# Kernel optimization log

Measured on AMD Instinct MI355X. Metric: run time of the kernel, lower is better.

The kernel has to match this reference:

```python
import jax, jax.numpy as jnp
import numpy as np

NEG_SLOPE = 0.2

def gatv2(x, edge_index, Wl, bl, Wr, br, att, bias):
    # PyG GATv2Conv (share_weights=False, add_self_loops=True, concat=True)
    N = x.shape[0]
    H, D = att.shape
    src0, dst0 = edge_index[0], edge_index[1]
    # remove_self_loops + add_self_loops semantics: mask existing self loops,
    # append one self loop per node (keeps static shapes under jit)
    loop = jnp.arange(N, dtype=src0.dtype)
    src = jnp.concatenate([src0, loop])
    dst = jnp.concatenate([dst0, loop])
    keep = jnp.concatenate([src0 != dst0, jnp.ones(N, dtype=bool)])  # drop original i->i edges
    xl = (x @ Wl + bl).reshape(N, H, D)  # source-side transform
    xr = (x @ Wr + br).reshape(N, H, D)  # target-side transform
    e = xl[src] + xr[dst]                                  # [E,H,D]
    logits = jnp.einsum('ehd,hd->eh', jax.nn.leaky_relu(e, NEG_SLOPE), att)
    logits = jnp.where(keep[:, None], logits, -jnp.inf)
    m = jax.ops.segment_max(logits, dst, num_segments=N)   # [N,H]
    ex = jnp.where(keep[:, None], jnp.exp(logits - m[dst]), 0.0)
    denom = jax.ops.segment_sum(ex, dst, num_segments=N)   # [N,H]
    alpha = ex / (denom[dst] + 1e-16)                      # [E,H]
    out = jax.ops.segment_sum(alpha[..., None] * xl[src], dst, num_segments=N)
    return out.reshape(N, H * D) + bias

def setup_inputs() -> dict:
    key = jax.random.key(0)
    ks = jax.random.split(key, 20)
    N, E, F, Hd = 50000, 400000, 5, 128
    s = 0.05
    inp = {
        'x': jax.random.normal(ks[0], (N, F), dtype=jnp.float32),
        'edge_index': jax.random.randint(ks[1], (2, E), 0, N, dtype=jnp.int64),
        # node_embed MLP
        'W1': jax.random.normal(ks[2], (F, Hd), dtype=jnp.float32) * s,
        'b1': jnp.zeros((Hd,), jnp.float32),
        'W2': jax.random.normal(ks[3], (Hd, Hd), dtype=jnp.float32) * s,
        'b2': jnp.zeros((Hd,), jnp.float32),
        # gnn1: GATv2Conv(128 -> 128, heads=4)
        'Wl1': jax.random.normal(ks[4], (Hd, 4 * Hd), dtype=jnp.float32) * s,
        'bl1': jnp.zeros((4 * Hd,), jnp.float32),
        'Wr1': jax.random.normal(ks[5], (Hd, 4 * Hd), dtype=jnp.float32) * s,
        'br1': jnp.zeros((4 * Hd,), jnp.float32),
        'att1': jax.random.normal(ks[6], (4, Hd), dtype=jnp.float32) * s,
        'bias1': jnp.zeros((4 * Hd,), jnp.float32),
        # gnn2: GATv2Conv(512 -> 128, heads=1)
        'Wl2': jax.random.normal(ks[7], (4 * Hd, Hd), dtype=jnp.float32) * s,
        'bl2': jnp.zeros((Hd,), jnp.float32),
        'Wr2': jax.random.normal(ks[8], (4 * Hd, Hd), dtype=jnp.float32) * s,
        'br2': jnp.zeros((Hd,), jnp.float32),
        'att2': jax.random.normal(ks[9], (1, Hd), dtype=jnp.float32) * s,
        'bias2': jnp.zeros((Hd,), jnp.float32),
    }
    return inp

def reference(x, edge_index, W1, b1, W2, b2, Wl1, bl1, Wr1, br1, att1, bias1,
              Wl2, bl2, Wr2, br2, att2, bias2):
    h = jax.nn.relu(x @ W1 + b1) @ W2 + b2                 # node_embed MLP
    h = jax.nn.relu(gatv2(h, edge_index, Wl1, bl1, Wr1, br1, att1, bias1))
    out = gatv2(h, edge_index, Wl2, bl2, Wr2, br2, att2, bias2)
    return out  # [N, 128]
```

## Files before the change

kernel.cpp:

```cpp
#include <hip/hip_runtime.h>
#include <math.h>

typedef __attribute__((ext_vector_type(8))) short bf16x8;
typedef __attribute__((ext_vector_type(4))) float f32x4;
typedef unsigned short ushort;

static __device__ __forceinline__ ushort f2bf(float f) {
    unsigned u = __float_as_uint(f);
    u = u + 0x7fff + ((u >> 16) & 1);
    return (ushort)(u >> 16);
}
static __device__ __forceinline__ float bf2f(ushort h) {
    return __uint_as_float(((unsigned)h) << 16);
}


__global__ void k_init(int* __restrict__ counts, int N) {
    int i = blockIdx.x * blockDim.x + threadIdx.x;
    if (i < N) counts[i] = 1;
}

__global__ void k_count(const int* __restrict__ src, const int* __restrict__ dst,
                        int E, int* __restrict__ counts) {
    int e = blockIdx.x * blockDim.x + threadIdx.x;
    if (e < E) {
        int s = src[e], d = dst[e];
        if (s != d) atomicAdd(&counts[d], 1);
    }
}

__global__ __launch_bounds__(256) void k_blocksum(const int* __restrict__ counts, int N,
                                                  int* __restrict__ bsum) {
    __shared__ int s[256];
    int t = threadIdx.x, i = blockIdx.x * 256 + t;
    s[t] = (i < N) ? counts[i] : 0;
    __syncthreads();
    for (int off = 128; off > 0; off >>= 1) {
        if (t < off) s[t] += s[t + off];
        __syncthreads();
    }
    if (t == 0) bsum[blockIdx.x] = s[0];
}

__global__ __launch_bounds__(256) void k_scanblocks(const int* __restrict__ bsum, int NB,
                                                    int* __restrict__ boff,
                                                    int* __restrict__ rowptr, int N) {
    __shared__ int s[256];
    int t = threadIdx.x;
    int v = (t < NB) ? bsum[t] : 0;
    s[t] = v;
    __syncthreads();
    for (int off = 1; off < 256; off <<= 1) {
        int u = (t >= off) ? s[t - off] : 0;
        __syncthreads();
        s[t] += u;
        __syncthreads();
    }
    if (t < NB) boff[t] = s[t] - v;
    if (t == NB - 1) rowptr[N] = s[t];
}

__global__ __launch_bounds__(256) void k_scatter(const int* __restrict__ counts, int N,
                                                 const int* __restrict__ boff,
                                                 int* __restrict__ rowptr,
                                                 int* __restrict__ cursor) {
    __shared__ int s[256];
    int t = threadIdx.x, i = blockIdx.x * 256 + t;
    int c = (i < N) ? counts[i] : 0;
    s[t] = c;
    __syncthreads();
    for (int off = 1; off < 256; off <<= 1) {
        int u = (t >= off) ? s[t - off] : 0;
        __syncthreads();
        s[t] += u;
        __syncthreads();
    }
    if (i < N) {
        int excl = boff[blockIdx.x] + s[t] - c;
        rowptr[i] = excl;
        cursor[i] = excl;
    }
}

__global__ void k_fill(const int* __restrict__ src, const int* __restrict__ dst,
                       int E, int N, int* __restrict__ cursor, int* __restrict__ colA) {
    int i = blockIdx.x * blockDim.x + threadIdx.x;
    if (i < E) {
        int s = src[i], d = dst[i];
        if (s != d) { int p = atomicAdd(&cursor[d], 1); colA[p] = s; }
    } else if (i < E + N) {
        int n = i - E;
        int p = atomicAdd(&cursor[n], 1); colA[p] = n;
    }
}


__global__ __launch_bounds__(256) void k_repack(
    const float* __restrict__ W2, const float* __restrict__ Wl1,
    const float* __restrict__ Wr1, const float* __restrict__ Wl2,
    const float* __restrict__ Wr2,
    ushort* __restrict__ wfh, ushort* __restrict__ wfl)
{
    int job = blockIdx.y;
    int t = blockIdx.x * 256 + threadIdx.x;
    int ks = t >> 9, n = (t >> 6) & 7, l = t & 63;

    const float* W; int ldw, rowoff, col0;
    if (job == 0)      { W = W2;  ldw = 128; rowoff = 0;              col0 = 0; }
    else if (job < 5)  { W = Wl1; ldw = 512; rowoff = 0;              col0 = (job - 1) * 128; }
    else if (job < 9)  { W = Wr1; ldw = 512; rowoff = 0;              col0 = (job - 5) * 128; }
    else if (job < 13) { W = Wl2; ldw = 128; rowoff = (job - 9) * 128;  col0 = 0; }
    else               { W = Wr2; ldw = 128; rowoff = (job - 13) * 128; col0 = 0; }

    int krow = rowoff + ks * 32 + (l >> 4) * 8;
    int col = col0 + n * 16 + (l & 15);
    size_t dbase = (size_t)job * 16384 + (((size_t)(ks * 8 + n)) * 64 + l) * 8;
#pragma unroll
    for (int j = 0; j < 8; j++) {
        float v = W[(size_t)(krow + j) * ldw + col];
        ushort h = f2bf(v);
        ushort lo = f2bf(v - bf2f(h));
        wfh[dbase + j] = h;
        wfl[dbase + j] = lo;
    }
}


__global__ __launch_bounds__(256) void k_mlp1(
    const float* __restrict__ x, const float* __restrict__ W1, const float* __restrict__ b1,
    ushort* __restrict__ outh, ushort* __restrict__ outl, int N)
{
    int n = blockIdx.x * 2 + (threadIdx.x >> 7);
    int j = threadIdx.x & 127;
    if (n >= N) return;
    float s = b1[j];
#pragma unroll
    for (int k = 0; k < 5; k++) s = fmaf(x[(size_t)n * 5 + k], W1[k * 128 + j], s);
    s = fmaxf(s, 0.f);
    ushort h = f2bf(s);
    outh[(size_t)n * 128 + j] = h;
    outl[(size_t)n * 128 + j] = f2bf(s - bf2f(h));
}


__global__ __launch_bounds__(256) void gemm_mfma(
    const ushort* __restrict__ Ah, const ushort* __restrict__ Al,
    const ushort* __restrict__ wfh, const ushort* __restrict__ wfl,
    const float* __restrict__ bias,
    ushort* __restrict__ Ch, ushort* __restrict__ Cl,
    int M)
{
    int tid = threadIdx.x;
    int w = tid >> 6, l = tid & 63;
    int m0 = blockIdx.x * 128 + w * 32;
    int lr = l & 15, kg = l >> 4;

    f32x4 acc[2][8];
#pragma unroll
    for (int i = 0; i < 2; i++)
#pragma unroll
        for (int j = 0; j < 8; j++) acc[i][j] = (f32x4){0.f, 0.f, 0.f, 0.f};

    int row0 = m0 + lr, row1 = m0 + 16 + lr;
    bool ok0 = row0 < M, ok1 = row1 < M;
    const bf16x8 zz = {0, 0, 0, 0, 0, 0, 0, 0};

#pragma unroll
    for (int ks = 0; ks < 4; ks++) {
        int koff = ks * 32 + kg * 8;
        bf16x8 a0h = ok0 ? *(const bf16x8*)(Ah + (size_t)row0 * 128 + koff) : zz;
        bf16x8 a0l = ok0 ? *(const bf16x8*)(Al + (size_t)row0 * 128 + koff) : zz;
        bf16x8 a1h = ok1 ? *(const bf16x8*)(Ah + (size_t)row1 * 128 + koff) : zz;
        bf16x8 a1l = ok1 ? *(const bf16x8*)(Al + (size_t)row1 * 128 + koff) : zz;
#pragma unroll
        for (int n = 0; n < 8; n++) {
            size_t bo = (((size_t)(ks * 8 + n)) * 64 + l) * 8;
            bf16x8 bh = *(const bf16x8*)(wfh + bo);
            bf16x8 bl = *(const bf16x8*)(wfl + bo);
            acc[0][n] = __builtin_amdgcn_mfma_f32_16x16x32_bf16(a0h, bh, acc[0][n], 0, 0, 0);
            acc[0][n] = __builtin_amdgcn_mfma_f32_16x16x32_bf16(a0h, bl, acc[0][n], 0, 0, 0);
            acc[0][n] = __builtin_amdgcn_mfma_f32_16x16x32_bf16(a0l, bh, acc[0][n], 0, 0, 0);
            acc[1][n] = __builtin_amdgcn_mfma_f32_16x16x32_bf16(a1h, bh, acc[1][n], 0, 0, 0);
            acc[1][n] = __builtin_amdgcn_mfma_f32_16x16x32_bf16(a1h, bl, acc[1][n], 0, 0, 0);
            acc[1][n] = __builtin_amdgcn_mfma_f32_16x16x32_bf16(a1l, bh, acc[1][n], 0, 0, 0);
        }
    }

#pragma unroll
    for (int mf = 0; mf < 2; mf++) {
#pragma unroll
        for (int r = 0; r < 4; r++) {
            int row = m0 + mf * 16 + kg * 4 + r;
            if (row >= M) continue;
#pragma unroll
            for (int n = 0; n < 8; n++) {
                size_t idx = (size_t)row * 128 + n * 16 + lr;
                float v = acc[mf][n][r] + bias[n * 16 + lr];
                ushort h = f2bf(v);
                Ch[idx] = h;
                Cl[idx] = f2bf(v - bf2f(h));
            }
        }
    }
}


__global__ __launch_bounds__(256) void gemm_xlr1(
    const ushort* __restrict__ Ah, const ushort* __restrict__ Al,
    const ushort* __restrict__ wh, const ushort* __restrict__ wl,
    const float* __restrict__ bl1, const float* __restrict__ br1,
    ushort* __restrict__ out, int M)
{
    __shared__ __align__(16) ushort Bh[16384];
    __shared__ __align__(16) ushort Bl[16384];

    int tid = threadIdx.x;
    int w = tid >> 6, l = tid & 63;
    int m0 = blockIdx.x * 128 + w * 32;
    int lr = l & 15, kg = l >> 4;

    int row0 = m0 + lr, row1 = m0 + 16 + lr;
    bool ok0 = row0 < M, ok1 = row1 < M;
    const bf16x8 zz = {0, 0, 0, 0, 0, 0, 0, 0};

    bf16x8 a0h[4], a0l[4], a1h[4], a1l[4];
#pragma unroll
    for (int ks = 0; ks < 4; ks++) {
        int koff = ks * 32 + kg * 8;
        a0h[ks] = ok0 ? *(const bf16x8*)(Ah + (size_t)row0 * 128 + koff) : zz;
        a0l[ks] = ok0 ? *(const bf16x8*)(Al + (size_t)row0 * 128 + koff) : zz;
        a1h[ks] = ok1 ? *(const bf16x8*)(Ah + (size_t)row1 * 128 + koff) : zz;
        a1l[ks] = ok1 ? *(const bf16x8*)(Al + (size_t)row1 * 128 + koff) : zz;
    }

    for (int t = 0; t < 8; t++) {
        __syncthreads();
        {
            const float4* gh = (const float4*)(wh + (size_t)t * 16384);
            const float4* gl = (const float4*)(wl + (size_t)t * 16384);
            float4* sh = (float4*)Bh;
            float4* sl = (float4*)Bl;
#pragma unroll
            for (int i = 0; i < 8; i++) {
                sh[i * 256 + tid] = gh[i * 256 + tid];
                sl[i * 256 + tid] = gl[i * 256 + tid];
            }
        }
        __syncthreads();

        f32x4 acc[2][8];
#pragma unroll
        for (int i = 0; i < 2; i++)
#pragma unroll
            for (int j = 0; j < 8; j++) acc[i][j] = (f32x4){0.f, 0.f, 0.f, 0.f};

#pragma unroll
        for (int ks = 0; ks < 4; ks++) {
#pragma unroll
            for (int n = 0; n < 8; n++) {
                int bo = ((ks * 8 + n) * 64 + l) * 8;
                bf16x8 bh = *(const bf16x8*)(Bh + bo);
                bf16x8 bl = *(const bf16x8*)(Bl + bo);
                acc[0][n] = __builtin_amdgcn_mfma_f32_16x16x32_bf16(a0h[ks], bh, acc[0][n], 0, 0, 0);
                acc[0][n] = __builtin_amdgcn_mfma_f32_16x16x32_bf16(a0h[ks], bl, acc[0][n], 0, 0, 0);
                acc[0][n] = __builtin_amdgcn_mfma_f32_16x16x32_bf16(a0l[ks], bh, acc[0][n], 0, 0, 0);
                acc[1][n] = __builtin_amdgcn_mfma_f32_16x16x32_bf16(a1h[ks], bh, acc[1][n], 0, 0, 0);
                acc[1][n] = __builtin_amdgcn_mfma_f32_16x16x32_bf16(a1h[ks], bl, acc[1][n], 0, 0, 0);
                acc[1][n] = __builtin_amdgcn_mfma_f32_16x16x32_bf16(a1l[ks], bh, acc[1][n], 0, 0, 0);
            }
        }

        float bcol[8];
#pragma unroll
        for (int n = 0; n < 8; n++)
            bcol[n] = (t < 4) ? bl1[t * 128 + n * 16 + lr] : br1[(t - 4) * 128 + n * 16 + lr];

#pragma unroll
        for (int mf = 0; mf < 2; mf++) {
#pragma unroll
            for (int r = 0; r < 4; r++) {
                int row = m0 + mf * 16 + kg * 4 + r;
                if (row >= M) continue;
#pragma unroll
                for (int n = 0; n < 8; n++)
                    out[(size_t)row * 1024 + t * 128 + n * 16 + lr] = f2bf(acc[mf][n][r] + bcol[n]);
            }
        }
    }
}


__global__ __launch_bounds__(256) void gemm_xlr2(
    const ushort* __restrict__ A,
    const ushort* __restrict__ wfh, const ushort* __restrict__ wfl,
    const float* __restrict__ bl2, const float* __restrict__ br2,
    ushort* __restrict__ xl2, ushort* __restrict__ xr2, int M)
{
    __shared__ __align__(16) ushort Bh[16384];
    __shared__ __align__(16) ushort Bl[16384];

    int tid = threadIdx.x;
    int w = tid >> 6, l = tid & 63;
    int m0 = blockIdx.x * 64 + w * 16;
    int lr = l & 15, kg = l >> 4;

    int row0 = m0 + lr;
    bool ok0 = row0 < M;
    const bf16x8 zz = {0, 0, 0, 0, 0, 0, 0, 0};

    f32x4 acc[2][8];
#pragma unroll
    for (int i = 0; i < 2; i++)
#pragma unroll
        for (int j = 0; j < 8; j++) acc[i][j] = (f32x4){0.f, 0.f, 0.f, 0.f};

    for (int kc = 0; kc < 4; kc++) {
        bf16x8 ah[4];
#pragma unroll
        for (int ks = 0; ks < 4; ks++)
            ah[ks] = ok0 ? *(const bf16x8*)(A + (size_t)row0 * 512 + kc * 128 + ks * 32 + kg * 8) : zz;

        for (int t = 0; t < 2; t++) {
            int slot = 9 + t * 4 + kc;
            __syncthreads();
            {
                const float4* gh = (const float4*)(wfh + (size_t)slot * 16384);
                const float4* gl = (const float4*)(wfl + (size_t)slot * 16384);
                float4* sh = (float4*)Bh;
                float4* sl = (float4*)Bl;
#pragma unroll
                for (int i = 0; i < 8; i++) {
                    sh[i * 256 + tid] = gh[i * 256 + tid];
                    sl[i * 256 + tid] = gl[i * 256 + tid];
                }
            }
            __syncthreads();
#pragma unroll
            for (int ks = 0; ks < 4; ks++) {
#pragma unroll
                for (int n = 0; n < 8; n++) {
                    int bo = ((ks * 8 + n) * 64 + l) * 8;
                    bf16x8 bh = *(const bf16x8*)(Bh + bo);
                    bf16x8 bl = *(const bf16x8*)(Bl + bo);
                    acc[t][n] = __builtin_amdgcn_mfma_f32_16x16x32_bf16(ah[ks], bh, acc[t][n], 0, 0, 0);
                    acc[t][n] = __builtin_amdgcn_mfma_f32_16x16x32_bf16(ah[ks], bl, acc[t][n], 0, 0, 0);
                }
            }
        }
    }

#pragma unroll
    for (int r = 0; r < 4; r++) {
        int row = m0 + kg * 4 + r;
        if (row >= M) continue;
#pragma unroll
        for (int n = 0; n < 8; n++) {
            int col = n * 16 + lr;
            xl2[(size_t)row * 128 + col] = f2bf(acc[0][n][r] + bl2[col]);
            xr2[(size_t)row * 128 + col] = f2bf(acc[1][n][r] + br2[col]);
        }
    }
}


__global__ __launch_bounds__(256) void gat_edge4(
    const ushort* __restrict__ xlr,
    const float* __restrict__ att,
    const float* __restrict__ bias,
    const int* __restrict__ rowptr, const int* __restrict__ colA,
    ushort* __restrict__ h1,
    int N)
{
    int n = blockIdx.x;
    int h = threadIdx.x >> 6, l = threadIdx.x & 63;
    int g = l >> 4, q = l & 15;
    const bf16x8 zz = {0, 0, 0, 0, 0, 0, 0, 0};

    bf16x8 xrv = *(const bf16x8*)(xlr + (size_t)n * 1024 + (4 + h) * 128 + q * 8);
    float xr[8], at[8];
#pragma unroll
    for (int j = 0; j < 8; j++) {
        xr[j] = bf2f((ushort)xrv[j]);
        at[j] = att[h * 128 + q * 8 + j];
    }

    int k0 = rowptr[n], k1 = rowptr[n + 1];
    float m = -INFINITY, s = 0.f;
    float o[8];
#pragma unroll
    for (int j = 0; j < 8; j++) o[j] = 0.f;

    int k = k0 + g;
    bf16x8 vv = zz;
    if (k < k1) {
        int srcn = colA[k];
        vv = *(const bf16x8*)(xlr + (size_t)srcn * 1024 + h * 128 + q * 8);
    }
    for (; k < k1; k += 4) {
        bf16x8 nv = zz;
        if (k + 4 < k1) {
            int ns = colA[k + 4];
            nv = *(const bf16x8*)(xlr + (size_t)ns * 1024 + h * 128 + q * 8);
        }
        float v[8], c = 0.f;
#pragma unroll
        for (int j = 0; j < 8; j++) {
            v[j] = bf2f((ushort)vv[j]);
            float t = v[j] + xr[j];
            t = (t > 0.f) ? t : 0.2f * t;
            c = fmaf(t, at[j], c);
        }
        c += __shfl_xor(c, 1);
        c += __shfl_xor(c, 2);
        c += __shfl_xor(c, 4);
        c += __shfl_xor(c, 8);
        if (c > m) {
            float sc = __expf(m - c);
            s *= sc;
#pragma unroll
            for (int j = 0; j < 8; j++) o[j] *= sc;
            m = c;
        }
        float p = __expf(c - m);
        s += p;
#pragma unroll
        for (int j = 0; j < 8; j++) o[j] = fmaf(p, v[j], o[j]);
        vv = nv;
    }

#pragma unroll
    for (int off = 16; off <= 32; off <<= 1) {
        float m2 = __shfl_xor(m, off);
        float s2 = __shfl_xor(s, off);
        float o2[8];
#pragma unroll
        for (int j = 0; j < 8; j++) o2[j] = __shfl_xor(o[j], off);
        float nm = fmaxf(m, m2);
        float fa = (m > -INFINITY) ? __expf(m - nm) : 0.f;
        float fb = (m2 > -INFINITY) ? __expf(m2 - nm) : 0.f;
        s = s * fa + s2 * fb;
#pragma unroll
        for (int j = 0; j < 8; j++) o[j] = o[j] * fa + o2[j] * fb;
        m = nm;
    }

    if (g == 0) {
        float inv = 1.f / (s + 1e-16f);
        bf16x8 pk;
#pragma unroll
        for (int j = 0; j < 8; j++) {
            float r = fmaxf(o[j] * inv + bias[h * 128 + q * 8 + j], 0.f);
            pk[j] = (short)f2bf(r);
        }
        *(bf16x8*)(h1 + (size_t)n * 512 + h * 128 + q * 8) = pk;
    }
}


__global__ __launch_bounds__(256) void gat_edge1(
    const ushort* __restrict__ xl, const ushort* __restrict__ xr,
    const float* __restrict__ att, const float* __restrict__ bias,
    const int* __restrict__ rowptr, const int* __restrict__ colA,
    float* __restrict__ out, int N)
{
    int n = blockIdx.x * 4 + (threadIdx.x >> 6);
    if (n >= N) return;
    int l = threadIdx.x & 63;
    int g = l >> 4, q = l & 15;
    const bf16x8 zz = {0, 0, 0, 0, 0, 0, 0, 0};

    bf16x8 xrv = *(const bf16x8*)(xr + (size_t)n * 128 + q * 8);
    float xrr[8], at[8];
#pragma unroll
    for (int j = 0; j < 8; j++) {
        xrr[j] = bf2f((ushort)xrv[j]);
        at[j] = att[q * 8 + j];
    }

    int k0 = rowptr[n], k1 = rowptr[n + 1];
    float m = -INFINITY, s = 0.f;
    float o[8];
#pragma unroll
    for (int j = 0; j < 8; j++) o[j] = 0.f;

    int k = k0 + g;
    bf16x8 vv = zz;
    if (k < k1) {
        int srcn = colA[k];
        vv = *(const bf16x8*)(xl + (size_t)srcn * 128 + q * 8);
    }
    for (; k < k1; k += 4) {
        bf16x8 nv = zz;
        if (k + 4 < k1) {
            int ns = colA[k + 4];
            nv = *(const bf16x8*)(xl + (size_t)ns * 128 + q * 8);
        }
        float v[8], c = 0.f;
#pragma unroll
        for (int j = 0; j < 8; j++) {
            v[j] = bf2f((ushort)vv[j]);
            float t = v[j] + xrr[j];
            t = (t > 0.f) ? t : 0.2f * t;
            c = fmaf(t, at[j], c);
        }
        c += __shfl_xor(c, 1);
        c += __shfl_xor(c, 2);
        c += __shfl_xor(c, 4);
        c += __shfl_xor(c, 8);
        if (c > m) {
            float sc = __expf(m - c);
            s *= sc;
#pragma unroll
            for (int j = 0; j < 8; j++) o[j] *= sc;
            m = c;
        }
        float p = __expf(c - m);
        s += p;
#pragma unroll
        for (int j = 0; j < 8; j++) o[j] = fmaf(p, v[j], o[j]);
        vv = nv;
    }

#pragma unroll
    for (int off = 16; off <= 32; off <<= 1) {
        float m2 = __shfl_xor(m, off);
        float s2 = __shfl_xor(s, off);
        float o2[8];
#pragma unroll
        for (int j = 0; j < 8; j++) o2[j] = __shfl_xor(o[j], off);
        float nm = fmaxf(m, m2);
        float fa = (m > -INFINITY) ? __expf(m - nm) : 0.f;
        float fb = (m2 > -INFINITY) ? __expf(m2 - nm) : 0.f;
        s = s * fa + s2 * fb;
#pragma unroll
        for (int j = 0; j < 8; j++) o[j] = o[j] * fa + o2[j] * fb;
        m = nm;
    }

    if (g == 0) {
        float inv = 1.f / (s + 1e-16f);
        float4 r0, r1;
        float* p0 = (float*)&r0; float* p1 = (float*)&r1;
#pragma unroll
        for (int j = 0; j < 4; j++) {
            p0[j] = o[j] * inv + bias[q * 8 + j];
            p1[j] = o[j + 4] * inv + bias[q * 8 + j + 4];
        }
        *(float4*)(out + (size_t)n * 128 + q * 8)     = r0;
        *(float4*)(out + (size_t)n * 128 + q * 8 + 4) = r1;
    }
}


extern "C" void kernel_launch(void* const* d_in, const int* in_sizes, int n_in,
                              void* d_out, int out_size, void* d_ws, size_t ws_size,
                              hipStream_t stream) {
    const float* x    = (const float*)d_in[0];
    const int* ei     = (const int*)d_in[1];
    const float* W1   = (const float*)d_in[2];
    const float* b1   = (const float*)d_in[3];
    const float* W2   = (const float*)d_in[4];
    const float* b2   = (const float*)d_in[5];
    const float* Wl1  = (const float*)d_in[6];
    const float* bl1  = (const float*)d_in[7];
    const float* Wr1  = (const float*)d_in[8];
    const float* br1  = (const float*)d_in[9];
    const float* att1 = (const float*)d_in[10];
    const float* bias1= (const float*)d_in[11];
    const float* Wl2  = (const float*)d_in[12];
    const float* bl2  = (const float*)d_in[13];
    const float* Wr2  = (const float*)d_in[14];
    const float* br2  = (const float*)d_in[15];
    const float* att2 = (const float*)d_in[16];
    const float* bias2= (const float*)d_in[17];

    int E = in_sizes[1] / 2;
    int N = in_sizes[0] / 5;
    const int* srcE = ei;
    const int* dstE = ei + E;

    float* dout = (float*)d_out;

    ushort* xlr1 = (ushort*)d_ws;
    ushort* h1   = xlr1 + (size_t)N * 1024;
    ushort* h0h  = h1 + (size_t)N * 512;
    ushort* h0l  = h0h + (size_t)N * 128;
    ushort* wfh  = h0l + (size_t)N * 128;
    ushort* wfl  = wfh + 17 * 16384;
    int* rowptr = (int*)(wfl + 17 * 16384);
    int* cursor = rowptr + (N + 1);
    int* counts = cursor + N;
    int* colA   = counts + N;
    int* bsum   = colA + (E + N);
    int* boff   = bsum + 256;

    ushort* cCh = h1;
    ushort* cCl = h1 + (size_t)N * 128;
    ushort* xl2 = h0h;
    ushort* xr2 = h0l;

    int NB = (N + 255) / 256;

    k_init <<<(N + 255) / 256, 256, 0, stream>>>(counts, N);
    k_count<<<(E + 255) / 256, 256, 0, stream>>>(srcE, dstE, E, counts);
    k_blocksum <<<NB, 256, 0, stream>>>(counts, N, bsum);
    k_scanblocks<<<1, 256, 0, stream>>>(bsum, NB, boff, rowptr, N);
    k_scatter  <<<NB, 256, 0, stream>>>(counts, N, boff, rowptr, cursor);
    k_fill <<<(E + N + 255) / 256, 256, 0, stream>>>(srcE, dstE, E, N, cursor, colA);

    {
        dim3 g(8, 17);
        k_repack<<<g, 256, 0, stream>>>(W2, Wl1, Wr1, Wl2, Wr2, wfh, wfl);
    }

    int mb128 = (N + 127) / 128;
    int mb64  = (N + 63) / 64;

    k_mlp1<<<(N + 1) / 2, 256, 0, stream>>>(x, W1, b1, cCh, cCl, N);
    gemm_mfma<<<mb128, 256, 0, stream>>>(cCh, cCl, wfh, wfl, b2, h0h, h0l, N);

    gemm_xlr1<<<mb128, 256, 0, stream>>>(h0h, h0l, wfh + 16384, wfl + 16384,
                                         bl1, br1, xlr1, N);
    gat_edge4<<<N, 256, 0, stream>>>(xlr1, att1, bias1, rowptr, colA, h1, N);

    gemm_xlr2<<<mb64, 256, 0, stream>>>(h1, wfh, wfl, bl2, br2, xl2, xr2, N);
    gat_edge1<<<(N + 3) / 4, 256, 0, stream>>>(xl2, xr2, att2, bias2, rowptr, colA, dout, N);
}
```

Before: 386.0 us.

## Drop low-part activation split, use self-loop logit as softmax shift, batch edge gathers

Activations feeding the first two GEMMs are now stored as a single bf16 array instead of a hi/lo pair, which removes one third of the MFMAs and half the activation traffic there. Both edge-attention kernels replace the online-softmax max tracking with a fixed shift equal to the self-loop logit, clamped at 80, so the rescaling branches and the max-merge in the final reduction go away. The edge loop now loads four neighbor rows at once per lane group to raise memory-level parallelism. In exchange, the activations lose the extra precision the lo part gave, and the fixed shift could underflow if a node's self logit is far above its other logits.

```diff
diff --git a/kernel.cpp b/kernel.cpp
--- a/kernel.cpp
+++ b/kernel.cpp
@@ -4,6 +4,7 @@
 typedef __attribute__((ext_vector_type(8))) short bf16x8;
 typedef __attribute__((ext_vector_type(4))) float f32x4;
 typedef unsigned short ushort;
+typedef unsigned int uint;
 
 static __device__ __forceinline__ ushort f2bf(float f) {
     unsigned u = __float_as_uint(f);
@@ -128,7 +129,7 @@
 
 __global__ __launch_bounds__(256) void k_mlp1(
     const float* __restrict__ x, const float* __restrict__ W1, const float* __restrict__ b1,
-    ushort* __restrict__ outh, ushort* __restrict__ outl, int N)
+    ushort* __restrict__ out, int N)
 {
     int n = blockIdx.x * 2 + (threadIdx.x >> 7);
     int j = threadIdx.x & 127;
@@ -137,18 +138,15 @@
 #pragma unroll
     for (int k = 0; k < 5; k++) s = fmaf(x[(size_t)n * 5 + k], W1[k * 128 + j], s);
     s = fmaxf(s, 0.f);
-    ushort h = f2bf(s);
-    outh[(size_t)n * 128 + j] = h;
-    outl[(size_t)n * 128 + j] = f2bf(s - bf2f(h));
-}
-
-
-__global__ __launch_bounds__(256) void gemm_mfma(
-    const ushort* __restrict__ Ah, const ushort* __restrict__ Al,
+    out[(size_t)n * 128 + j] = f2bf(s);
+}
+
+
+__global__ __launch_bounds__(256) void gemm_h0(
+    const ushort* __restrict__ A,
     const ushort* __restrict__ wfh, const ushort* __restrict__ wfl,
     const float* __restrict__ bias,
-    ushort* __restrict__ Ch, ushort* __restrict__ Cl,
-    int M)
+    ushort* __restrict__ C, int M)
 {
     int tid = threadIdx.x;
     int w = tid >> 6, l = tid & 63;
@@ -168,21 +166,17 @@
 #pragma unroll
     for (int ks = 0; ks < 4; ks++) {
         int koff = ks * 32 + kg * 8;
-        bf16x8 a0h = ok0 ? *(const bf16x8*)(Ah + (size_t)row0 * 128 + koff) : zz;
-        bf16x8 a0l = ok0 ? *(const bf16x8*)(Al + (size_t)row0 * 128 + koff) : zz;
-        bf16x8 a1h = ok1 ? *(const bf16x8*)(Ah + (size_t)row1 * 128 + koff) : zz;
-        bf16x8 a1l = ok1 ? *(const bf16x8*)(Al + (size_t)row1 * 128 + koff) : zz;
+        bf16x8 a0 = ok0 ? *(const bf16x8*)(A + (size_t)row0 * 128 + koff) : zz;
+        bf16x8 a1 = ok1 ? *(const bf16x8*)(A + (size_t)row1 * 128 + koff) : zz;
 #pragma unroll
         for (int n = 0; n < 8; n++) {
             size_t bo = (((size_t)(ks * 8 + n)) * 64 + l) * 8;
             bf16x8 bh = *(const bf16x8*)(wfh + bo);
             bf16x8 bl = *(const bf16x8*)(wfl + bo);
-            acc[0][n] = __builtin_amdgcn_mfma_f32_16x16x32_bf16(a0h, bh, acc[0][n], 0, 0, 0);
-            acc[0][n] = __builtin_amdgcn_mfma_f32_16x16x32_bf16(a0h, bl, acc[0][n], 0, 0, 0);
-            acc[0][n] = __builtin_amdgcn_mfma_f32_16x16x32_bf16(a0l, bh, acc[0][n], 0, 0, 0);
-            acc[1][n] = __builtin_amdgcn_mfma_f32_16x16x32_bf16(a1h, bh, acc[1][n], 0, 0, 0);
-            acc[1][n] = __builtin_amdgcn_mfma_f32_16x16x32_bf16(a1h, bl, acc[1][n], 0, 0, 0);
-            acc[1][n] = __builtin_amdgcn_mfma_f32_16x16x32_bf16(a1l, bh, acc[1][n], 0, 0, 0);
+            acc[0][n] = __builtin_amdgcn_mfma_f32_16x16x32_bf16(a0, bh, acc[0][n], 0, 0, 0);
+            acc[0][n] = __builtin_amdgcn_mfma_f32_16x16x32_bf16(a0, bl, acc[0][n], 0, 0, 0);
+            acc[1][n] = __builtin_amdgcn_mfma_f32_16x16x32_bf16(a1, bh, acc[1][n], 0, 0, 0);
+            acc[1][n] = __builtin_amdgcn_mfma_f32_16x16x32_bf16(a1, bl, acc[1][n], 0, 0, 0);
         }
     }
 
@@ -195,10 +189,7 @@
 #pragma unroll
             for (int n = 0; n < 8; n++) {
                 size_t idx = (size_t)row * 128 + n * 16 + lr;
-                float v = acc[mf][n][r] + bias[n * 16 + lr];
-                ushort h = f2bf(v);
-                Ch[idx] = h;
-                Cl[idx] = f2bf(v - bf2f(h));
+                C[idx] = f2bf(acc[mf][n][r] + bias[n * 16 + lr]);
             }
         }
     }
@@ -206,7 +197,7 @@
 
 
 __global__ __launch_bounds__(256) void gemm_xlr1(
-    const ushort* __restrict__ Ah, const ushort* __restrict__ Al,
+    const ushort* __restrict__ A,
     const ushort* __restrict__ wh, const ushort* __restrict__ wl,
     const float* __restrict__ bl1, const float* __restrict__ br1,
     ushort* __restrict__ out, int M)
@@ -223,14 +214,12 @@
     bool ok0 = row0 < M, ok1 = row1 < M;
     const bf16x8 zz = {0, 0, 0, 0, 0, 0, 0, 0};
 
-    bf16x8 a0h[4], a0l[4], a1h[4], a1l[4];
+    bf16x8 a0[4], a1[4];
 #pragma unroll
     for (int ks = 0; ks < 4; ks++) {
         int koff = ks * 32 + kg * 8;
-        a0h[ks] = ok0 ? *(const bf16x8*)(Ah + (size_t)row0 * 128 + koff) : zz;
-        a0l[ks] = ok0 ? *(const bf16x8*)(Al + (size_t)row0 * 128 + koff) : zz;
-        a1h[ks] = ok1 ? *(const bf16x8*)(Ah + (size_t)row1 * 128 + koff) : zz;
-        a1l[ks] = ok1 ? *(const bf16x8*)(Al + (size_t)row1 * 128 + koff) : zz;
+        a0[ks] = ok0 ? *(const bf16x8*)(A + (size_t)row0 * 128 + koff) : zz;
+        a1[ks] = ok1 ? *(const bf16x8*)(A + (size_t)row1 * 128 + koff) : zz;
     }
 
     for (int t = 0; t < 8; t++) {
@@ -261,12 +250,10 @@
                 int bo = ((ks * 8 + n) * 64 + l) * 8;
                 bf16x8 bh = *(const bf16x8*)(Bh + bo);
                 bf16x8 bl = *(const bf16x8*)(Bl + bo);
-                acc[0][n] = __builtin_amdgcn_mfma_f32_16x16x32_bf16(a0h[ks], bh, acc[0][n], 0, 0, 0);
-                acc[0][n] = __builtin_amdgcn_mfma_f32_16x16x32_bf16(a0h[ks], bl, acc[0][n], 0, 0, 0);
-                acc[0][n] = __builtin_amdgcn_mfma_f32_16x16x32_bf16(a0l[ks], bh, acc[0][n], 0, 0, 0);
-                acc[1][n] = __builtin_amdgcn_mfma_f32_16x16x32_bf16(a1h[ks], bh, acc[1][n], 0, 0, 0);
-                acc[1][n] = __builtin_amdgcn_mfma_f32_16x16x32_bf16(a1h[ks], bl, acc[1][n], 0, 0, 0);
-                acc[1][n] = __builtin_amdgcn_mfma_f32_16x16x32_bf16(a1l[ks], bh, acc[1][n], 0, 0, 0);
+                acc[0][n] = __builtin_amdgcn_mfma_f32_16x16x32_bf16(a0[ks], bh, acc[0][n], 0, 0, 0);
+                acc[0][n] = __builtin_amdgcn_mfma_f32_16x16x32_bf16(a0[ks], bl, acc[0][n], 0, 0, 0);
+                acc[1][n] = __builtin_amdgcn_mfma_f32_16x16x32_bf16(a1[ks], bh, acc[1][n], 0, 0, 0);
+                acc[1][n] = __builtin_amdgcn_mfma_f32_16x16x32_bf16(a1[ks], bl, acc[1][n], 0, 0, 0);
             }
         }
 
@@ -374,39 +361,22 @@
     int n = blockIdx.x;
     int h = threadIdx.x >> 6, l = threadIdx.x & 63;
     int g = l >> 4, q = l & 15;
-    const bf16x8 zz = {0, 0, 0, 0, 0, 0, 0, 0};
+
+    const ushort* xlbase = xlr + h * 128 + q * 8;
 
     bf16x8 xrv = *(const bf16x8*)(xlr + (size_t)n * 1024 + (4 + h) * 128 + q * 8);
-    float xr[8], at[8];
-#pragma unroll
-    for (int j = 0; j < 8; j++) {
-        xr[j] = bf2f((ushort)xrv[j]);
-        at[j] = att[h * 128 + q * 8 + j];
-    }
-
-    int k0 = rowptr[n], k1 = rowptr[n + 1];
-    float m = -INFINITY, s = 0.f;
-    float o[8];
-#pragma unroll
-    for (int j = 0; j < 8; j++) o[j] = 0.f;
-
-    int k = k0 + g;
-    bf16x8 vv = zz;
-    if (k < k1) {
-        int srcn = colA[k];
-        vv = *(const bf16x8*)(xlr + (size_t)srcn * 1024 + h * 128 + q * 8);
-    }
-    for (; k < k1; k += 4) {
-        bf16x8 nv = zz;
-        if (k + 4 < k1) {
-            int ns = colA[k + 4];
-            nv = *(const bf16x8*)(xlr + (size_t)ns * 1024 + h * 128 + q * 8);
-        }
-        float v[8], c = 0.f;
+    float4 ata = *(const float4*)(att + h * 128 + q * 8);
+    float4 atb = *(const float4*)(att + h * 128 + q * 8 + 4);
+    float xr[8] , at[8] = {ata.x, ata.y, ata.z, ata.w, atb.x, atb.y, atb.z, atb.w};
+#pragma unroll
+    for (int j = 0; j < 8; j++) xr[j] = bf2f((ushort)xrv[j]);
+
+    auto dotc = [&](bf16x8 v8, float* vv) -> float {
+        float c = 0.f;
 #pragma unroll
         for (int j = 0; j < 8; j++) {
-            v[j] = bf2f((ushort)vv[j]);
-            float t = v[j] + xr[j];
+            vv[j] = bf2f((ushort)v8[j]);
+            float t = vv[j] + xr[j];
             t = (t > 0.f) ? t : 0.2f * t;
             c = fmaf(t, at[j], c);
         }
@@ -414,44 +384,61 @@
         c += __shfl_xor(c, 2);
         c += __shfl_xor(c, 4);
         c += __shfl_xor(c, 8);
-        if (c > m) {
-            float sc = __expf(m - c);
-            s *= sc;
-#pragma unroll
-            for (int j = 0; j < 8; j++) o[j] *= sc;
-            m = c;
-        }
-        float p = __expf(c - m);
+        return c;
+    };
+
+    float tmp[8];
+    bf16x8 vself = *(const bf16x8*)(xlbase + (size_t)n * 1024);
+    float cs = dotc(vself, tmp);
+
+    int k0 = rowptr[n], k1 = rowptr[n + 1];
+    float s = 0.f, o[8];
+#pragma unroll
+    for (int j = 0; j < 8; j++) o[j] = 0.f;
+
+    auto edge = [&](bf16x8 v8) {
+        float vv[8];
+        float c = dotc(v8, vv);
+        float p = __expf(fminf(c - cs, 80.f));
         s += p;
 #pragma unroll
-        for (int j = 0; j < 8; j++) o[j] = fmaf(p, v[j], o[j]);
-        vv = nv;
+        for (int j = 0; j < 8; j++) o[j] = fmaf(p, vv[j], o[j]);
+    };
+
+    for (int base = k0 + g; base < k1; base += 16) {
+        int x0 = colA[base];
+        int x1 = (base + 4  < k1) ? colA[base + 4]  : -1;
+        int x2 = (base + 8  < k1) ? colA[base + 8]  : -1;
+        int x3 = (base + 12 < k1) ? colA[base + 12] : -1;
+        int y1 = (x1 >= 0) ? x1 : n;
+        int y2 = (x2 >= 0) ? x2 : n;
+        int y3 = (x3 >= 0) ? x3 : n;
+        bf16x8 v0 = *(const bf16x8*)(xlbase + (size_t)x0 * 1024);
+        bf16x8 v1 = *(const bf16x8*)(xlbase + (size_t)y1 * 1024);
+        bf16x8 v2 = *(const bf16x8*)(xlbase + (size_t)y2 * 1024);
+        bf16x8 v3 = *(const bf16x8*)(xlbase + (size_t)y3 * 1024);
+        edge(v0);
+        if (x1 >= 0) edge(v1);
+        if (x2 >= 0) edge(v2);
+        if (x3 >= 0) edge(v3);
     }
 
 #pragma unroll
     for (int off = 16; off <= 32; off <<= 1) {
-        float m2 = __shfl_xor(m, off);
-        float s2 = __shfl_xor(s, off);
-        float o2[8];
-#pragma unroll
-        for (int j = 0; j < 8; j++) o2[j] = __shfl_xor(o[j], off);
-        float nm = fmaxf(m, m2);
-        float fa = (m > -INFINITY) ? __expf(m - nm) : 0.f;
-        float fb = (m2 > -INFINITY) ? __expf(m2 - nm) : 0.f;
-        s = s * fa + s2 * fb;
-#pragma unroll
-        for (int j = 0; j < 8; j++) o[j] = o[j] * fa + o2[j] * fb;
-        m = nm;
+        s += __shfl_xor(s, off);
+#pragma unroll
+        for (int j = 0; j < 8; j++) o[j] += __shfl_xor(o[j], off);
     }
 
     if (g == 0) {
         float inv = 1.f / (s + 1e-16f);
+        float4 ba = *(const float4*)(bias + h * 128 + q * 8);
+        float4 bb = *(const float4*)(bias + h * 128 + q * 8 + 4);
+        float bs[8] = {ba.x, ba.y, ba.z, ba.w, bb.x, bb.y, bb.z, bb.w};
         bf16x8 pk;
 #pragma unroll
-        for (int j = 0; j < 8; j++) {
-            float r = fmaxf(o[j] * inv + bias[h * 128 + q * 8 + j], 0.f);
-            pk[j] = (short)f2bf(r);
-        }
+        for (int j = 0; j < 8; j++)
+            pk[j] = (short)f2bf(fmaxf(o[j] * inv + bs[j], 0.f));
         *(bf16x8*)(h1 + (size_t)n * 512 + h * 128 + q * 8) = pk;
     }
 }
@@ -467,39 +454,22 @@
     if (n >= N) return;
     int l = threadIdx.x & 63;
     int g = l >> 4, q = l & 15;
-    const bf16x8 zz = {0, 0, 0, 0, 0, 0, 0, 0};
+
+    const ushort* xlbase = xl + q * 8;
 
     bf16x8 xrv = *(const bf16x8*)(xr + (size_t)n * 128 + q * 8);
-    float xrr[8], at[8];
-#pragma unroll
-    for (int j = 0; j < 8; j++) {
-        xrr[j] = bf2f((ushort)xrv[j]);
-        at[j] = att[q * 8 + j];
-    }
-
-    int k0 = rowptr[n], k1 = rowptr[n + 1];
-    float m = -INFINITY, s = 0.f;
-    float o[8];
-#pragma unroll
-    for (int j = 0; j < 8; j++) o[j] = 0.f;
-
-    int k = k0 + g;
-    bf16x8 vv = zz;
-    if (k < k1) {
-        int srcn = colA[k];
-        vv = *(const bf16x8*)(xl + (size_t)srcn * 128 + q * 8);
-    }
-    for (; k < k1; k += 4) {
-        bf16x8 nv = zz;
-        if (k + 4 < k1) {
-            int ns = colA[k + 4];
-            nv = *(const bf16x8*)(xl + (size_t)ns * 128 + q * 8);
-        }
-        float v[8], c = 0.f;
+    float4 ata = *(const float4*)(att + q * 8);
+    float4 atb = *(const float4*)(att + q * 8 + 4);
+    float xrr[8], at[8] = {ata.x, ata.y, ata.z, ata.w, atb.x, atb.y, atb.z, atb.w};
+#pragma unroll
+    for (int j = 0; j < 8; j++) xrr[j] = bf2f((ushort)xrv[j]);
+
+    auto dotc = [&](bf16x8 v8, float* vv) -> float {
+        float c = 0.f;
 #pragma unroll
         for (int j = 0; j < 8; j++) {
-            v[j] = bf2f((ushort)vv[j]);
-            float t = v[j] + xrr[j];
+            vv[j] = bf2f((ushort)v8[j]);
+            float t = vv[j] + xrr[j];
             t = (t > 0.f) ? t : 0.2f * t;
             c = fmaf(t, at[j], c);
         }
@@ -507,45 +477,61 @@
         c += __shfl_xor(c, 2);
         c += __shfl_xor(c, 4);
         c += __shfl_xor(c, 8);
-        if (c > m) {
-            float sc = __expf(m - c);
-            s *= sc;
-#pragma unroll
-            for (int j = 0; j < 8; j++) o[j] *= sc;
-            m = c;
-        }
-        float p = __expf(c - m);
+        return c;
+    };
+
+    float tmp[8];
+    bf16x8 vself = *(const bf16x8*)(xlbase + (size_t)n * 128);
+    float cs = dotc(vself, tmp);
+
+    int k0 = rowptr[n], k1 = rowptr[n + 1];
+    float s = 0.f, o[8];
+#pragma unroll
+    for (int j = 0; j < 8; j++) o[j] = 0.f;
+
+    auto edge = [&](bf16x8 v8) {
+        float vv[8];
+        float c = dotc(v8, vv);
+        float p = __expf(fminf(c - cs, 80.f));
         s += p;
 #pragma unroll
-        for (int j = 0; j < 8; j++) o[j] = fmaf(p, v[j], o[j]);
-        vv = nv;
+        for (int j = 0; j < 8; j++) o[j] = fmaf(p, vv[j], o[j]);
+    };
+
+    for (int base = k0 + g; base < k1; base += 16) {
+        int x0 = colA[base];
+        int x1 = (base + 4  < k1) ? colA[base + 4]  : -1;
+        int x2 = (base + 8  < k1) ? colA[base + 8]  : -1;
+        int x3 = (base + 12 < k1) ? colA[base + 12] : -1;
+        int y1 = (x1 >= 0) ? x1 : n;
+        int y2 = (x2 >= 0) ? x2 : n;
+        int y3 = (x3 >= 0) ? x3 : n;
+        bf16x8 v0 = *(const bf16x8*)(xlbase + (size_t)x0 * 128);
+        bf16x8 v1 = *(const bf16x8*)(xlbase + (size_t)y1 * 128);
+        bf16x8 v2 = *(const bf16x8*)(xlbase + (size_t)y2 * 128);
+        bf16x8 v3 = *(const bf16x8*)(xlbase + (size_t)y3 * 128);
+        edge(v0);
+        if (x1 >= 0) edge(v1);
+        if (x2 >= 0) edge(v2);
+        if (x3 >= 0) edge(v3);
     }
 
 #pragma unroll
     for (int off = 16; off <= 32; off <<= 1) {
-        float m2 = __shfl_xor(m, off);
-        float s2 = __shfl_xor(s, off);
-        float o2[8];
-#pragma unroll
-        for (int j = 0; j < 8; j++) o2[j] = __shfl_xor(o[j], off);
-        float nm = fmaxf(m, m2);
-        float fa = (m > -INFINITY) ? __expf(m - nm) : 0.f;
-        float fb = (m2 > -INFINITY) ? __expf(m2 - nm) : 0.f;
-        s = s * fa + s2 * fb;
-#pragma unroll
-        for (int j = 0; j < 8; j++) o[j] = o[j] * fa + o2[j] * fb;
-        m = nm;
+        s += __shfl_xor(s, off);
+#pragma unroll
+        for (int j = 0; j < 8; j++) o[j] += __shfl_xor(o[j], off);
     }
 
     if (g == 0) {
         float inv = 1.f / (s + 1e-16f);
+        float4 ba = *(const float4*)(bias + q * 8);
+        float4 bb = *(const float4*)(bias + q * 8 + 4);
         float4 r0, r1;
-        float* p0 = (float*)&r0; float* p1 = (float*)&r1;
-#pragma unroll
-        for (int j = 0; j < 4; j++) {
-            p0[j] = o[j] * inv + bias[q * 8 + j];
-            p1[j] = o[j + 4] * inv + bias[q * 8 + j + 4];
-        }
+        r0.x = o[0] * inv + ba.x;  r0.y = o[1] * inv + ba.y;
+        r0.z = o[2] * inv + ba.z;  r0.w = o[3] * inv + ba.w;
+        r1.x = o[4] * inv + bb.x;  r1.y = o[5] * inv + bb.y;
+        r1.z = o[6] * inv + bb.z;  r1.w = o[7] * inv + bb.w;
         *(float4*)(out + (size_t)n * 128 + q * 8)     = r0;
         *(float4*)(out + (size_t)n * 128 + q * 8 + 4) = r1;
     }
@@ -583,9 +569,9 @@
 
     ushort* xlr1 = (ushort*)d_ws;
     ushort* h1   = xlr1 + (size_t)N * 1024;
-    ushort* h0h  = h1 + (size_t)N * 512;
-    ushort* h0l  = h0h + (size_t)N * 128;
-    ushort* wfh  = h0l + (size_t)N * 128;
+    ushort* h0   = h1 + (size_t)N * 512;
+    ushort* xr2  = h0 + (size_t)N * 128;
+    ushort* wfh  = xr2 + (size_t)N * 128;
     ushort* wfl  = wfh + 17 * 16384;
     int* rowptr = (int*)(wfl + 17 * 16384);
     int* cursor = rowptr + (N + 1);
@@ -594,10 +580,8 @@
     int* bsum   = colA + (E + N);
     int* boff   = bsum + 256;
 
-    ushort* cCh = h1;
-    ushort* cCl = h1 + (size_t)N * 128;
-    ushort* xl2 = h0h;
-    ushort* xr2 = h0l;
+    ushort* cC  = h1;
+    ushort* xl2 = h0;
 
     int NB = (N + 255) / 256;
 
@@ -616,10 +600,10 @@
     int mb128 = (N + 127) / 128;
     int mb64  = (N + 63) / 64;
 
-    k_mlp1<<<(N + 1) / 2, 256, 0, stream>>>(x, W1, b1, cCh, cCl, N);
-    gemm_mfma<<<mb128, 256, 0, stream>>>(cCh, cCl, wfh, wfl, b2, h0h, h0l, N);
-
-    gemm_xlr1<<<mb128, 256, 0, stream>>>(h0h, h0l, wfh + 16384, wfl + 16384,
+    k_mlp1<<<(N + 1) / 2, 256, 0, stream>>>(x, W1, b1, cC, N);
+    gemm_h0<<<mb128, 256, 0, stream>>>(cC, wfh, wfl, b2, h0, N);
+
+    gemm_xlr1<<<mb128, 256, 0, stream>>>(h0, wfh + 16384, wfl + 16384,
                                          bl1, br1, xlr1, N);
     gat_edge4<<<N, 256, 0, stream>>>(xlr1, att1, bias1, rowptr, colA, h1, N);
 
```

Result: no change. 380.0 us (-1.6%).
